# Kernel tuning notes

Measured on AMD Instinct MI355X. Metric: run time of the kernel, lower is better.

The kernel has to match this reference:

```python
import jax, jax.numpy as jnp
import numpy as np

N_NODES = 100000
N_EDGES = 800000
HIDDEN = 128


def setup_inputs() -> dict:
    key = jax.random.key(0)
    k1, k2, k3, k4, k5, k6 = jax.random.split(key, 6)
    z = jax.random.normal(k1, (N_NODES, HIDDEN), dtype=jnp.float32)
    edge_index = jax.random.randint(k2, (2, N_EDGES), 0, N_NODES, dtype=jnp.int64)
    # nn.Linear params (torch default init scale ~ 1/sqrt(fan_in))
    s1 = 1.0 / np.sqrt(2 * HIDDEN)
    s2 = 1.0 / np.sqrt(HIDDEN)
    W1 = jax.random.uniform(k3, (2 * HIDDEN, HIDDEN), jnp.float32, -s1, s1)
    b1 = jax.random.uniform(k4, (HIDDEN,), jnp.float32, -s1, s1)
    W2 = jax.random.uniform(k5, (HIDDEN, 1), jnp.float32, -s2, s2)
    b2 = jax.random.uniform(k6, (1,), jnp.float32, -s2, s2)
    return {"z": z, "edge_index": edge_index, "W1": W1, "b1": b1, "W2": W2, "b2": b2}


def reference(z, edge_index, W1, b1, W2, b2):
    src, dst = edge_index[0], edge_index[1]
    # Gather endpoint features: [E, H] each. Avoid materializing the [E, 2H]
    # concat by splitting W1 into src/dst halves (same math as cat + matmul).
    W1_src, W1_dst = W1[:HIDDEN], W1[HIDDEN:]
    h = z[src] @ W1_src + z[dst] @ W1_dst + b1  # [E, H]
    h = jax.nn.relu(h)
    score = h @ W2 + b2  # [E, 1]
    return score
```

## Files before the change

kernel.cpp:

```cpp
#include <hip/hip_runtime.h>
#include <hip/hip_bf16.h>

#define N_NODES 100000
#define N_EDGES 800000
#define HIDDEN 128
#define NGROUPS 6250
#define PC_BLOCKS 512
#define PC_STRIDE 2048

typedef short frag_ab __attribute__((ext_vector_type(8)));
typedef float frag_cd __attribute__((ext_vector_type(4)));

__device__ inline unsigned short f2b(float f) {
    union { float f; unsigned u; } x; x.f = f;
    return (unsigned short)((x.u + 0x7fffu + ((x.u >> 16) & 1u)) >> 16);
}

__device__ inline unsigned pk2(float x, float y) {
    union { __hip_bfloat162 h; unsigned u; } c;
    c.h = __float22bfloat162_rn(make_float2(x, y));
    return c.u;
}

__global__ __launch_bounds__(256) void transpose_w1(
    const float* __restrict__ W1, unsigned short* __restrict__ Bt)
{
    const int t  = threadIdx.x;
    const int nc = blockIdx.x * 4 + (t >> 6);
    const int k2 = (t & 63) * 2;
    const int col  = nc & 127;
    const int roff = (nc >= 128) ? 128 : 0;
    float f0 = W1[(size_t)(roff + k2)     * HIDDEN + col];
    float f1 = W1[(size_t)(roff + k2 + 1) * HIDDEN + col];
    *(unsigned*)(Bt + (size_t)nc * HIDDEN + k2) = (unsigned)f2b(f0) | ((unsigned)f2b(f1) << 16);
}

__global__ __launch_bounds__(256) void precompute_uv_mfma(
    const float* __restrict__ z, const unsigned short* __restrict__ Bt,
    const float* __restrict__ b1, unsigned char* __restrict__ UVq,
    float* __restrict__ scales)
{
    __shared__ unsigned short smem[4096 * 8];
    const int t = threadIdx.x;
    const int lane = t & 63;
    const int w = t >> 6;
    const int g  = lane >> 4;
    const int lc = lane & 15;

    {
        const uint4* bt4 = (const uint4*)Bt;
        uint4* s4 = (uint4*)smem;
        #pragma unroll
        for (int k = 0; k < 16; ++k)
            s4[k * 256 + t] = bt4[t * 16 + k];
    }
    __syncthreads();

    const float4* zbase = (const float4*)z;
    const float4* b1f4  = (const float4*)b1;
    const frag_ab* wlds = (const frag_ab*)smem;

    int gid = blockIdx.x * 4 + w;
    float4 cur[8];
    {
        const float4* zrow = zbase + (size_t)(gid * 16 + lc) * 32;
        #pragma unroll
        for (int i = 0; i < 8; ++i)
            cur[i] = zrow[(i >> 1) * 8 + g * 2 + (i & 1)];
    }

    while (true) {
        frag_ab zf[4];
        #pragma unroll
        for (int q = 0; q < 4; ++q) {
            union { unsigned u[4]; frag_ab f; } pk;
            pk.u[0] = pk2(cur[q * 2].x,     cur[q * 2].y);
            pk.u[1] = pk2(cur[q * 2].z,     cur[q * 2].w);
            pk.u[2] = pk2(cur[q * 2 + 1].x, cur[q * 2 + 1].y);
            pk.u[3] = pk2(cur[q * 2 + 1].z, cur[q * 2 + 1].w);
            zf[q] = pk.f;
        }

        const int nxt = gid + PC_STRIDE;
        const bool have = (nxt < NGROUPS);
        if (have) {
            const float4* zrow = zbase + (size_t)(nxt * 16 + lc) * 32;
            #pragma unroll
            for (int i = 0; i < 8; ++i)
                cur[i] = zrow[(i >> 1) * 8 + g * 2 + (i & 1)];
        }

        frag_cd acc[16];
        #pragma unroll
        for (int mt = 0; mt < 16; ++mt)
            acc[mt] = (frag_cd){0.f, 0.f, 0.f, 0.f};
        #pragma unroll
        for (int q = 0; q < 4; ++q) {
            #pragma unroll
            for (int mt = 0; mt < 16; ++mt) {
                frag_ab wf = wlds[(q * 4 + g) * 256 + mt * 16 + lc];
                acc[mt] = __builtin_amdgcn_mfma_f32_16x16x32_bf16(wf, zf[q], acc[mt], 0, 0, 0);
            }
        }

        float mxU = 0.f, mxV = 0.f;
        #pragma unroll
        for (int mt = 0; mt < 8; ++mt) {
            float4 bb = b1f4[mt * 4 + g];
            acc[mt][0] += bb.x; acc[mt][1] += bb.y;
            acc[mt][2] += bb.z; acc[mt][3] += bb.w;
            #pragma unroll
            for (int r = 0; r < 4; ++r)
                mxU = fmaxf(mxU, fabsf(acc[mt][r]));
        }
        #pragma unroll
        for (int mt = 8; mt < 16; ++mt)
            #pragma unroll
            for (int r = 0; r < 4; ++r)
                mxV = fmaxf(mxV, fabsf(acc[mt][r]));

        mxU = fmaxf(mxU, __shfl_xor(mxU, 16));
        mxU = fmaxf(mxU, __shfl_xor(mxU, 32));
        mxV = fmaxf(mxV, __shfl_xor(mxV, 16));
        mxV = fmaxf(mxV, __shfl_xor(mxV, 32));
        mxU = fmaxf(mxU, 1e-12f);
        mxV = fmaxf(mxV, 1e-12f);
        const float ainvU = 127.0f / mxU;
        const float ainvV = 127.0f / mxV;

        const int node = gid * 16 + lc;
        unsigned char* urow = UVq + (size_t)node * 256;
        #pragma unroll
        for (int mt = 0; mt < 16; ++mt) {
            const float ainv = (mt < 8) ? ainvU : ainvV;
            unsigned q0 = (unsigned)__builtin_fmaf(acc[mt][0], ainv, 128.5f);
            unsigned q1 = (unsigned)__builtin_fmaf(acc[mt][1], ainv, 128.5f);
            unsigned q2 = (unsigned)__builtin_fmaf(acc[mt][2], ainv, 128.5f);
            unsigned q3 = (unsigned)__builtin_fmaf(acc[mt][3], ainv, 128.5f);
            *(unsigned*)&urow[mt * 16 + g * 4] = q0 | (q1 << 8) | (q2 << 16) | (q3 << 24);
        }
        if (g == 0) {
            scales[node * 2 + 0] = mxU * (1.0f / 127.0f);
            scales[node * 2 + 1] = mxV * (1.0f / 127.0f);
        }

        if (!have) break;
        gid = nxt;
    }
}

__device__ inline float dq4(unsigned uq, unsigned vq, float aU, float aV,
                            float k, float4 w, float acc) {
    #pragma unroll
    for (int b = 0; b < 4; ++b) {
        float uf = (float)((uq >> (8 * b)) & 0xffu);
        float vf = (float)((vq >> (8 * b)) & 0xffu);
        float h  = __builtin_fmaf(aU, uf, __builtin_fmaf(aV, vf, k));
        h = fmaxf(h, 0.f);
        float wv = (b == 0) ? w.x : (b == 1) ? w.y : (b == 2) ? w.z : w.w;
        acc = __builtin_fmaf(h, wv, acc);
    }
    return acc;
}

__global__ __launch_bounds__(256) void edge_score(
    const int* __restrict__ ei, const unsigned char* __restrict__ UVq,
    const float* __restrict__ scales, const float* __restrict__ W2,
    const float* __restrict__ B2, float* __restrict__ out)
{
    const int t = threadIdx.x;
    const int g = t & 7;
    const int slot = t >> 3;
    const int e0 = blockIdx.x * 64 + slot;
    const int e1 = e0 + 32;

    const float4* W24 = (const float4*)W2;
    const float4 w0 = W24[g * 4 + 0];
    const float4 w1 = W24[g * 4 + 1];
    const float4 w2 = W24[g * 4 + 2];
    const float4 w3 = W24[g * 4 + 3];

    const int s0 = ei[e0];
    const int d0 = ei[N_EDGES + e0];
    const int s1 = ei[e1];
    const int d1 = ei[N_EDGES + e1];

    const uint4 u0 = *(const uint4*)(UVq + (size_t)s0 * 256 + g * 16);
    const uint4 v0 = *(const uint4*)(UVq + (size_t)d0 * 256 + 128 + g * 16);
    const uint4 u1 = *(const uint4*)(UVq + (size_t)s1 * 256 + g * 16);
    const uint4 v1 = *(const uint4*)(UVq + (size_t)d1 * 256 + 128 + g * 16);
    const float aU0 = scales[s0 * 2];
    const float aV0 = scales[d0 * 2 + 1];
    const float aU1 = scales[s1 * 2];
    const float aV1 = scales[d1 * 2 + 1];

    const float k0 = -128.f * (aU0 + aV0);
    const float k1 = -128.f * (aU1 + aV1);

    float A = 0.f, B = 0.f;
    A = dq4(u0.x, v0.x, aU0, aV0, k0, w0, A);
    A = dq4(u0.y, v0.y, aU0, aV0, k0, w1, A);
    A = dq4(u0.z, v0.z, aU0, aV0, k0, w2, A);
    A = dq4(u0.w, v0.w, aU0, aV0, k0, w3, A);

    B = dq4(u1.x, v1.x, aU1, aV1, k1, w0, B);
    B = dq4(u1.y, v1.y, aU1, aV1, k1, w1, B);
    B = dq4(u1.z, v1.z, aU1, aV1, k1, w2, B);
    B = dq4(u1.w, v1.w, aU1, aV1, k1, w3, B);

    float sa = A;
    float sb = B;
    sa += __shfl_xor(sa, 1, 8);
    sa += __shfl_xor(sa, 2, 8);
    sa += __shfl_xor(sa, 4, 8);
    sb += __shfl_xor(sb, 1, 8);
    sb += __shfl_xor(sb, 2, 8);
    sb += __shfl_xor(sb, 4, 8);

    if (g == 0) {
        float bb = B2[0];
        out[e0] = sa + bb;
        out[e1] = sb + bb;
    }
}

extern "C" void kernel_launch(void* const* d_in, const int* in_sizes, int n_in,
                              void* d_out, int out_size, void* d_ws, size_t ws_size,
                              hipStream_t stream) {
    const float* z  = (const float*)d_in[0];
    const int*   ei = (const int*)d_in[1];
    const float* W1 = (const float*)d_in[2];
    const float* b1 = (const float*)d_in[3];
    const float* W2 = (const float*)d_in[4];
    const float* b2 = (const float*)d_in[5];
    float* out = (float*)d_out;

    unsigned char* UVq = (unsigned char*)d_ws;
    float* scales = (float*)(UVq + (size_t)N_NODES * 256);
    unsigned short* Bt = (unsigned short*)(scales + 2 * N_NODES);

    transpose_w1<<<64, 256, 0, stream>>>(W1, Bt);
    precompute_uv_mfma<<<PC_BLOCKS, 256, 0, stream>>>(z, Bt, b1, UVq, scales);
    edge_score<<<N_EDGES / 64, 256, 0, stream>>>(ei, UVq, scales, W2, b2, out);
}
```

Before: 143.3 us.

## Fuse W1 transpose into precompute kernel and widen blocks to 512 threads

Drops the separate transpose_w1 launch. Each precompute block now reads W1 directly from global memory, converts it to bf16 and writes it into LDS itself. Blocks grow to 8 waves and the grid stride doubles, so each wave handles fewer groups, and the register prefetch of the next z tile is removed. This saves a kernel launch and the intermediate Bt buffer, in exchange for redundant strided W1 reads in all 512 blocks and no software prefetch overlap.

```diff
diff --git a/kernel.cpp b/kernel.cpp
--- a/kernel.cpp
+++ b/kernel.cpp
@@ -6,7 +6,7 @@
 #define HIDDEN 128
 #define NGROUPS 6250
 #define PC_BLOCKS 512
-#define PC_STRIDE 2048
+#define PC_STRIDE 4096
 
 typedef short frag_ab __attribute__((ext_vector_type(8)));
 typedef float frag_cd __attribute__((ext_vector_type(4)));
@@ -22,21 +22,8 @@
     return c.u;
 }
 
-__global__ __launch_bounds__(256) void transpose_w1(
-    const float* __restrict__ W1, unsigned short* __restrict__ Bt)
-{
-    const int t  = threadIdx.x;
-    const int nc = blockIdx.x * 4 + (t >> 6);
-    const int k2 = (t & 63) * 2;
-    const int col  = nc & 127;
-    const int roff = (nc >= 128) ? 128 : 0;
-    float f0 = W1[(size_t)(roff + k2)     * HIDDEN + col];
-    float f1 = W1[(size_t)(roff + k2 + 1) * HIDDEN + col];
-    *(unsigned*)(Bt + (size_t)nc * HIDDEN + k2) = (unsigned)f2b(f0) | ((unsigned)f2b(f1) << 16);
-}
-
-__global__ __launch_bounds__(256) void precompute_uv_mfma(
-    const float* __restrict__ z, const unsigned short* __restrict__ Bt,
+__global__ __launch_bounds__(512) void precompute_uv_mfma(
+    const float* __restrict__ z, const float* __restrict__ W1,
     const float* __restrict__ b1, unsigned char* __restrict__ UVq,
     float* __restrict__ scales)
 {
@@ -48,11 +35,23 @@
     const int lc = lane & 15;
 
     {
-        const uint4* bt4 = (const uint4*)Bt;
-        uint4* s4 = (uint4*)smem;
-        #pragma unroll
-        for (int k = 0; k < 16; ++k)
-            s4[k * 256 + t] = bt4[t * 16 + k];
+        const int r    = t & 255;
+        const int jj   = t >> 8;
+        const int roff = (r >= 128) ? 128 : 0;
+        const int col  = r & 127;
+        #pragma unroll
+        for (int sl = 0; sl < 8; ++sl) {
+            const int s = jj * 8 + sl;
+            unsigned u[4];
+            #pragma unroll
+            for (int p = 0; p < 4; ++p) {
+                float f0 = W1[(size_t)(roff + s * 8 + p * 2)     * HIDDEN + col];
+                float f1 = W1[(size_t)(roff + s * 8 + p * 2 + 1) * HIDDEN + col];
+                u[p] = (unsigned)f2b(f0) | ((unsigned)f2b(f1) << 16);
+            }
+            uint4* dst = (uint4*)&smem[(size_t)(s * 256 + r) * 8];
+            *dst = make_uint4(u[0], u[1], u[2], u[3]);
+        }
     }
     __syncthreads();
 
@@ -60,16 +59,14 @@
     const float4* b1f4  = (const float4*)b1;
     const frag_ab* wlds = (const frag_ab*)smem;
 
-    int gid = blockIdx.x * 4 + w;
-    float4 cur[8];
-    {
+    int gid = blockIdx.x * 8 + w;
+    while (true) {
         const float4* zrow = zbase + (size_t)(gid * 16 + lc) * 32;
+        float4 cur[8];
         #pragma unroll
         for (int i = 0; i < 8; ++i)
             cur[i] = zrow[(i >> 1) * 8 + g * 2 + (i & 1)];
-    }
-
-    while (true) {
+
         frag_ab zf[4];
         #pragma unroll
         for (int q = 0; q < 4; ++q) {
@@ -79,15 +76,6 @@
             pk.u[2] = pk2(cur[q * 2 + 1].x, cur[q * 2 + 1].y);
             pk.u[3] = pk2(cur[q * 2 + 1].z, cur[q * 2 + 1].w);
             zf[q] = pk.f;
-        }
-
-        const int nxt = gid + PC_STRIDE;
-        const bool have = (nxt < NGROUPS);
-        if (have) {
-            const float4* zrow = zbase + (size_t)(nxt * 16 + lc) * 32;
-            #pragma unroll
-            for (int i = 0; i < 8; ++i)
-                cur[i] = zrow[(i >> 1) * 8 + g * 2 + (i & 1)];
         }
 
         frag_cd acc[16];
@@ -144,8 +132,8 @@
             scales[node * 2 + 1] = mxV * (1.0f / 127.0f);
         }
 
-        if (!have) break;
-        gid = nxt;
+        gid += PC_STRIDE;
+        if (gid >= NGROUPS) break;
     }
 }
 
@@ -237,9 +225,7 @@
 
     unsigned char* UVq = (unsigned char*)d_ws;
     float* scales = (float*)(UVq + (size_t)N_NODES * 256);
-    unsigned short* Bt = (unsigned short*)(scales + 2 * N_NODES);
-
-    transpose_w1<<<64, 256, 0, stream>>>(W1, Bt);
-    precompute_uv_mfma<<<PC_BLOCKS, 256, 0, stream>>>(z, Bt, b1, UVq, scales);
+
+    precompute_uv_mfma<<<PC_BLOCKS, 512, 0, stream>>>(z, W1, b1, UVq, scales);
     edge_score<<<N_EDGES / 64, 256, 0, stream>>>(ei, UVq, scales, W2, b2, out);
 }
```

Result: slower. 228.2 us (+59.2%).
